# Kernel optimization log

Measured on AMD Instinct MI355X. Metric: run time of the kernel, lower is better.

Reference implementation:

```python
import jax, jax.numpy as jnp
import numpy as np

B, S, D, F, E, K = 4, 2048, 512, 1024, 8, 2

def setup_inputs() -> dict:
    key = jax.random.key(0)
    ks = jax.random.split(key, 7)
    hidden = jax.random.normal(ks[0], (B, S, D), dtype=jnp.float32)
    top_k_indices = jax.random.randint(ks[1], (B, S, K), 0, E, dtype=jnp.int32)
    top_k_weights = jax.random.uniform(ks[2], (B, S, K), dtype=jnp.float32)
    scale1 = 1.0 / np.sqrt(D)
    scale2 = 1.0 / np.sqrt(F)
    W1 = jax.random.normal(ks[3], (E, D, F), dtype=jnp.float32) * scale1
    b1 = jnp.zeros((E, F), dtype=jnp.float32)
    W2 = jax.random.normal(ks[4], (E, F, D), dtype=jnp.float32) * scale2
    b2 = jnp.zeros((E, D), dtype=jnp.float32)
    return {"hidden": hidden, "top_k_indices": top_k_indices,
            "top_k_weights": top_k_weights, "W1": W1, "b1": b1, "W2": W2, "b2": b2}

def reference(hidden, top_k_indices, top_k_weights, W1, b1, W2, b2):
    b, s, d = hidden.shape
    e = W1.shape[0]
    x = hidden.reshape(-1, d)                      # [T, D]
    idx = top_k_indices.reshape(-1, top_k_indices.shape[-1])   # [T, K]
    w = top_k_weights.reshape(-1, top_k_weights.shape[-1])     # [T, K]
    # combine weight per (token, expert): sum over k slots routed to expert e
    onehot = jax.nn.one_hot(idx, e, dtype=w.dtype)             # [T, K, E]
    cw = jnp.einsum('tk,tke->et', w, onehot)                   # [E, T]
    def step(acc, params):
        W1e, b1e, W2e, b2e, cwe = params
        h = jax.nn.gelu(x @ W1e + b1e)                         # [T, F]
        y = h @ W2e + b2e                                      # [T, D]
        return acc + cwe[:, None] * y, None
    out, _ = jax.lax.scan(step, jnp.zeros_like(x), (W1, b1, W2, b2, cw))
    return out.reshape(b, s, d)
```

## Files before the change

kernel.cpp:

```cpp
#include <hip/hip_runtime.h>
#include <hip/hip_bf16.h>

#define T_TOK 8192
#define DDIM  512
#define FDIM  1024
#define NEXP  8
#define KTOP  2
#define NSLOT (T_TOK * KTOP)
#define MAX_ROWS 17408
#define MAX_T128 136

typedef __attribute__((ext_vector_type(8))) __bf16 bf16x8;
typedef __attribute__((ext_vector_type(4))) __bf16 bf16x4;
typedef __attribute__((ext_vector_type(4))) float  f32x4;
typedef __attribute__((ext_vector_type(8))) unsigned short u16x8;

typedef __attribute__((address_space(1))) const unsigned int* gp1;
typedef __attribute__((address_space(3))) unsigned int*       lp3;
#define GL2LDS(g, l) __builtin_amdgcn_global_load_lds((gp1)(const void*)(g), (lp3)(void*)(l), 16, 0, 0)


__device__ __forceinline__ float gelu_fast(float x){
    float u = 0.7978845608028654f * (x + 0.044715f * x * x * x);
    return x / (1.0f + __expf(-2.0f * u));
}

__device__ __forceinline__ unsigned short f2bf(float v){
    __hip_bfloat16 b = __float2bfloat16(v);
    return *(unsigned short*)&b;
}

__global__ void cast_x_bf16(const float* __restrict__ src, unsigned short* __restrict__ dst,
                            int n8){
    int i = blockIdx.x * blockDim.x + threadIdx.x;
    if (i >= n8) return;
    const float4* s = (const float4*)src;
    float4 a = s[2 * i];
    float4 b = s[2 * i + 1];
    u16x8 o;
    o[0] = f2bf(a.x); o[1] = f2bf(a.y); o[2] = f2bf(a.z); o[3] = f2bf(a.w);
    o[4] = f2bf(b.x); o[5] = f2bf(b.y); o[6] = f2bf(b.z); o[7] = f2bf(b.w);
    *(u16x8*)(dst + (size_t)i * 8) = o;
}

__global__ __launch_bounds__(1024) void bucket_kernel(
    const int* __restrict__ idx, int* __restrict__ meta, int2* __restrict__ map,
    int* __restrict__ list, int* __restrict__ slot2row)
{
    __shared__ unsigned long long sA[1024], sB[1024];
    const int tid = threadIdx.x;
    const int base = tid * 16;

    int mye[16];
    unsigned long long a = 0, b = 0;
    #pragma unroll
    for (int i = 0; i < 16; i++){
        int e = idx[base + i] & 7;
        mye[i] = e;
        unsigned long long one = 1ull << (16 * (e & 3));
        if (e < 4) a += one; else b += one;
    }
    sA[tid] = a; sB[tid] = b;
    __syncthreads();

    for (int off = 1; off < 1024; off <<= 1){
        unsigned long long ta = 0, tb = 0;
        if (tid >= off){ ta = sA[tid - off]; tb = sB[tid - off]; }
        __syncthreads();
        sA[tid] += ta; sB[tid] += tb;
        __syncthreads();
    }

    const unsigned long long iA = sA[tid],  iB = sB[tid];
    const unsigned long long tA = sA[1023], tB = sB[1023];

    int cnt[NEXP], pad[NEXP], off_e[NEXP], tc[NEXP + 1];
    tc[0] = 0;
    int o = 0;
    #pragma unroll
    for (int e = 0; e < NEXP; e++){
        unsigned long long src = (e < 4) ? tA : tB;
        cnt[e] = (int)((src >> (16 * (e & 3))) & 0xffffull);
        pad[e] = (cnt[e] + 127) & ~127;
        off_e[e] = o; o += pad[e];
        tc[e + 1] = tc[e] + (pad[e] >> 7);
    }
    const int nrows = o, nt = tc[NEXP];

    if (tid == 0) meta[16] = nt;
    if (tid < NEXP) meta[17 + tid] = off_e[tid];
    if (tid < nt){
        int e = 0;
        while (tid >= tc[e + 1]) e++;
        map[tid] = make_int2(e, off_e[e] + (tid - tc[e]) * 128);
    }

    int run[NEXP];
    #pragma unroll
    for (int e = 0; e < NEXP; e++){
        unsigned long long isrc = (e < 4) ? iA : iB;
        unsigned long long csrc = (e < 4) ? a  : b;
        int incl = (int)((isrc >> (16 * (e & 3))) & 0xffffull);
        int ce   = (int)((csrc >> (16 * (e & 3))) & 0xffffull);
        run[e] = off_e[e] + incl - ce;
    }
    #pragma unroll
    for (int i = 0; i < 16; i++){
        int e = mye[i];
        int gg = run[e]++;
        list[gg] = (base + i) >> 1;
        slot2row[base + i] = gg;
    }

    for (int p = tid; p < nrows; p += 1024){
        #pragma unroll
        for (int e = 0; e < NEXP; e++){
            if (p >= off_e[e] + cnt[e] && p < off_e[e] + pad[e]) list[p] = 0;
        }
    }
}

__global__ void transpose_cast(const float* __restrict__ src,
                               unsigned short* __restrict__ dst, int R, int C){
    __shared__ unsigned short tile[32][33];
    int e = blockIdx.z;
    int c0 = blockIdx.x * 32, r0 = blockIdx.y * 32;
    int tx = threadIdx.x, ty = threadIdx.y;
    const float* sf = src + (size_t)e * R * C;
    unsigned short* d = dst + (size_t)e * R * C;
    #pragma unroll
    for (int i = 0; i < 4; i++)
        tile[ty + i * 8][tx] = f2bf(sf[(size_t)(r0 + ty + i * 8) * C + c0 + tx]);
    __syncthreads();
    #pragma unroll
    for (int i = 0; i < 4; i++)
        d[(size_t)(c0 + ty + i * 8) * R + r0 + tx] = tile[tx][ty + i * 8];
}

#define PIPE_PROLOGUE_SYNC()  do {                                   \
    asm volatile("s_waitcnt vmcnt(0)" ::: "memory");                 \
    __builtin_amdgcn_s_barrier();                                    \
    __builtin_amdgcn_sched_barrier(0);                               \
} while (0)
#define PIPE_STEP_SYNC()  do {                                       \
    __builtin_amdgcn_sched_barrier(0);                               \
    asm volatile("s_waitcnt vmcnt(0) lgkmcnt(0)" ::: "memory");      \
    __builtin_amdgcn_s_barrier();                                    \
    __builtin_amdgcn_sched_barrier(0);                               \
} while (0)

__global__ __launch_bounds__(256, 2) void gemm1_kernel(
    const unsigned short* __restrict__ x,
    const unsigned short* __restrict__ w1t,
    const float* __restrict__ b1,
    const int* __restrict__ meta,
    const int2* __restrict__ map,
    const int* __restrict__ list,
    unsigned short* __restrict__ h)
{
    const int ntiles = meta[16];
    const int nwg = ntiles * (FDIM / 128);
    int id = blockIdx.y * gridDim.x + blockIdx.x;
    if (id >= nwg) return;
    int q = nwg >> 3, r = nwg & 7;
    int xcd = id & 7, rank = id >> 3;
    int swz = (xcd < r) ? (xcd * (q + 1) + rank)
                        : (r * (q + 1) + (xcd - r) * q + rank);
    const int tile = swz >> 3;
    const int n0 = (swz & 7) * 128;
    int2 em = map[tile];
    const int e = em.x, grow0 = em.y;

    __shared__ __align__(16) unsigned short As[2][8192];
    __shared__ __align__(16) unsigned short Bs[2][8192];

    const int tid  = threadIdx.x;
    const int wave = tid >> 6;
    const int lane = tid & 63;
    const int rl   = lane >> 2;
    const int kq   = lane & 3;

    const int row0 = wave * 16 + rl;
    const int row1 = 64 + wave * 16 + rl;

    const unsigned short* pA0 = x + (size_t)list[grow0 + row0] * DDIM + kq * 8;
    const unsigned short* pA1 = x + (size_t)list[grow0 + row1] * DDIM + kq * 8;
    const unsigned short* pB0 = w1t + ((size_t)e * FDIM + n0 + row0) * DDIM + kq * 8;
    const unsigned short* pB1 = w1t + ((size_t)e * FDIM + n0 + row1) * DDIM + kq * 8;

    const int quad = lane >> 4, lrow = lane & 15;
    const int wr = (wave >> 1) * 64;
    const int wc = (wave & 1) * 64;

#define STAGE1(buf, kk) do {                                                  \
        char* la_ = (char*)As[buf] + wave * 1024;                             \
        char* lb_ = (char*)Bs[buf] + wave * 1024;                             \
        GL2LDS(pA0 + (kk),      la_);          GL2LDS(pA1 + (kk),      la_ + 4096);  \
        GL2LDS(pA0 + (kk) + 32, la_ + 8192);   GL2LDS(pA1 + (kk) + 32, la_ + 12288); \
        GL2LDS(pB0 + (kk),      lb_);          GL2LDS(pB1 + (kk),      lb_ + 4096);  \
        GL2LDS(pB0 + (kk) + 32, lb_ + 8192);   GL2LDS(pB1 + (kk) + 32, lb_ + 12288); \
    } while (0)

    f32x4 acc[4][4];
    #pragma unroll
    for (int i = 0; i < 4; i++)
        #pragma unroll
        for (int j = 0; j < 4; j++) acc[i][j] = (f32x4)0.0f;

    STAGE1(0, 0);
    PIPE_PROLOGUE_SYNC();

    const int NK = DDIM / 64;
    #pragma unroll 2
    for (int t = 0; t < NK; ++t){
        const int cur = t & 1;
        if (t + 1 < NK) STAGE1(cur ^ 1, (t + 1) * 64);
        bf16x8 a[4][2], b[4][2];
        #pragma unroll
        for (int i = 0; i < 4; i++){
            #pragma unroll
            for (int ks = 0; ks < 2; ks++){
                a[i][ks] = *(const bf16x8*)&As[cur][ks * 4096 + (wr + i * 16 + lrow) * 32 + quad * 8];
                b[i][ks] = *(const bf16x8*)&Bs[cur][ks * 4096 + (wc + i * 16 + lrow) * 32 + quad * 8];
            }
        }
        #pragma unroll
        for (int i = 0; i < 4; i++){
            #pragma unroll
            for (int j = 0; j < 4; j++){
                acc[i][j] = __builtin_amdgcn_mfma_f32_16x16x32_bf16(a[i][0], b[j][0], acc[i][j], 0, 0, 0);
                acc[i][j] = __builtin_amdgcn_mfma_f32_16x16x32_bf16(a[i][1], b[j][1], acc[i][j], 0, 0, 0);
            }
        }
        if (t + 1 < NK) PIPE_STEP_SYNC();
    }
#undef STAGE1

    #pragma unroll
    for (int j = 0; j < 4; j++){
        int cn = n0 + wc + j * 16 + lrow;
        float bias = b1[e * FDIM + cn];
        #pragma unroll
        for (int i = 0; i < 4; i++){
            #pragma unroll
            for (int rr = 0; rr < 4; rr++){
                int gr = grow0 + wr + i * 16 + quad * 4 + rr;
                h[(size_t)gr * FDIM + cn] = f2bf(gelu_fast(acc[i][j][rr] + bias));
            }
        }
    }
}

__global__ __launch_bounds__(256, 2) void gemm2_kernel(
    const unsigned short* __restrict__ h,
    const unsigned short* __restrict__ w2t,
    const float* __restrict__ b2,
    const int* __restrict__ meta,
    const int2* __restrict__ map,
    unsigned short* __restrict__ y)
{
    const int ntiles = meta[16];
    const int nwg = ntiles * (DDIM / 128);
    int id = blockIdx.y * gridDim.x + blockIdx.x;
    if (id >= nwg) return;
    int q = nwg >> 3, r = nwg & 7;
    int xcd = id & 7, rank = id >> 3;
    int swz = (xcd < r) ? (xcd * (q + 1) + rank)
                        : (r * (q + 1) + (xcd - r) * q + rank);
    const int tile = swz >> 2;
    const int n0 = (swz & 3) * 128;
    int2 em = map[tile];
    const int e = em.x, grow0 = em.y;

    __shared__ __align__(16) unsigned short As[2][8192];
    __shared__ __align__(16) unsigned short Bs[2][8192];

    const int tid  = threadIdx.x;
    const int wave = tid >> 6;
    const int lane = tid & 63;
    const int rl   = lane >> 2;
    const int kq   = lane & 3;

    const int row0 = wave * 16 + rl;
    const int row1 = 64 + wave * 16 + rl;

    const unsigned short* pA0 = h + (size_t)(grow0 + row0) * FDIM + kq * 8;
    const unsigned short* pA1 = h + (size_t)(grow0 + row1) * FDIM + kq * 8;
    const unsigned short* pB0 = w2t + ((size_t)e * DDIM + n0 + row0) * FDIM + kq * 8;
    const unsigned short* pB1 = w2t + ((size_t)e * DDIM + n0 + row1) * FDIM + kq * 8;

    const int quad = lane >> 4, lrow = lane & 15;
    const int wr = (wave >> 1) * 64;
    const int wc = (wave & 1) * 64;

#define STAGE2(buf, kk) do {                                                  \
        char* la_ = (char*)As[buf] + wave * 1024;                             \
        char* lb_ = (char*)Bs[buf] + wave * 1024;                             \
        GL2LDS(pA0 + (kk),      la_);          GL2LDS(pA1 + (kk),      la_ + 4096);  \
        GL2LDS(pA0 + (kk) + 32, la_ + 8192);   GL2LDS(pA1 + (kk) + 32, la_ + 12288); \
        GL2LDS(pB0 + (kk),      lb_);          GL2LDS(pB1 + (kk),      lb_ + 4096);  \
        GL2LDS(pB0 + (kk) + 32, lb_ + 8192);   GL2LDS(pB1 + (kk) + 32, lb_ + 12288); \
    } while (0)

    f32x4 acc[4][4];
    #pragma unroll
    for (int i = 0; i < 4; i++)
        #pragma unroll
        for (int j = 0; j < 4; j++) acc[i][j] = (f32x4)0.0f;

    STAGE2(0, 0);
    PIPE_PROLOGUE_SYNC();

    const int NK = FDIM / 64;
    #pragma unroll 2
    for (int t = 0; t < NK; ++t){
        const int cur = t & 1;
        if (t + 1 < NK) STAGE2(cur ^ 1, (t + 1) * 64);
        bf16x8 a[4][2], b[4][2];
        #pragma unroll
        for (int i = 0; i < 4; i++){
            #pragma unroll
            for (int ks = 0; ks < 2; ks++){
                a[i][ks] = *(const bf16x8*)&As[cur][ks * 4096 + (wr + i * 16 + lrow) * 32 + quad * 8];
                b[i][ks] = *(const bf16x8*)&Bs[cur][ks * 4096 + (wc + i * 16 + lrow) * 32 + quad * 8];
            }
        }
        #pragma unroll
        for (int i = 0; i < 4; i++){
            #pragma unroll
            for (int j = 0; j < 4; j++){
                acc[i][j] = __builtin_amdgcn_mfma_f32_16x16x32_bf16(a[i][0], b[j][0], acc[i][j], 0, 0, 0);
                acc[i][j] = __builtin_amdgcn_mfma_f32_16x16x32_bf16(a[i][1], b[j][1], acc[i][j], 0, 0, 0);
            }
        }
        if (t + 1 < NK) PIPE_STEP_SYNC();
    }
#undef STAGE2

    #pragma unroll
    for (int j = 0; j < 4; j++){
        int cn = n0 + wc + j * 16 + lrow;
        float bias = b2[e * DDIM + cn];
        #pragma unroll
        for (int i = 0; i < 4; i++){
            #pragma unroll
            for (int rr = 0; rr < 4; rr++){
                int gr = grow0 + wr + i * 16 + quad * 4 + rr;
                y[(size_t)gr * DDIM + cn] = f2bf(acc[i][j][rr] + bias);
            }
        }
    }
}

__global__ void combine_kernel(const unsigned short* __restrict__ y,
                               const int* __restrict__ slot2row,
                               const float* __restrict__ wk,
                               float* __restrict__ out){
    int g = blockIdx.x * blockDim.x + threadIdx.x;
    int t = g >> 7, seg = g & 127;
    int ra = slot2row[2 * t], rb = slot2row[2 * t + 1];
    float wa = wk[2 * t];
    float wb = wk[2 * t + 1];
    bf16x4 ya = *(const bf16x4*)(y + (size_t)ra * DDIM + seg * 4);
    bf16x4 yb = *(const bf16x4*)(y + (size_t)rb * DDIM + seg * 4);
    float4 o;
    o.x = wa * (float)ya[0] + wb * (float)yb[0];
    o.y = wa * (float)ya[1] + wb * (float)yb[1];
    o.z = wa * (float)ya[2] + wb * (float)yb[2];
    o.w = wa * (float)ya[3] + wb * (float)yb[3];
    *(float4*)(out + (size_t)t * DDIM + seg * 4) = o;
}

extern "C" void kernel_launch(void* const* d_in, const int* in_sizes, int n_in,
                              void* d_out, int out_size, void* d_ws, size_t ws_size,
                              hipStream_t stream){
    const float* x   = (const float*)d_in[0];
    const int*   idx = (const int*)d_in[1];
    const float* wk  = (const float*)d_in[2];
    const float* W1  = (const float*)d_in[3];
    const float* b1  = (const float*)d_in[4];
    const float* W2  = (const float*)d_in[5];
    const float* b2  = (const float*)d_in[6];
    float* out = (float*)d_out;

    char* ws = (char*)d_ws;
    int*   meta     = (int*)ws;
    int2*  map      = (int2*)(ws + 512);
    int*   list     = (int*)(ws + 4096);
    int*   slot2row = (int*)(ws + 81920);
    unsigned short* xbf = (unsigned short*)(ws + 262144);
    unsigned short* w1t = (unsigned short*)(ws + 8650752);
    unsigned short* w2t = (unsigned short*)(ws + 17039360);
    unsigned short* h   = (unsigned short*)(ws + 25427968);
    unsigned short* y   = (unsigned short*)(ws + 61079552);
    if (ws_size < 78905344u) return;

    cast_x_bf16<<<(T_TOK * DDIM / 8) / 256, 256, 0, stream>>>(x, xbf, T_TOK * DDIM / 8);

    transpose_cast<<<dim3(FDIM / 32, DDIM / 32, NEXP), dim3(32, 8), 0, stream>>>(
        W1, w1t, DDIM, FDIM);
    transpose_cast<<<dim3(DDIM / 32, FDIM / 32, NEXP), dim3(32, 8), 0, stream>>>(
        W2, w2t, FDIM, DDIM);

    bucket_kernel<<<1, 1024, 0, stream>>>(idx, meta, map, list, slot2row);

    gemm1_kernel<<<dim3(FDIM / 128, MAX_T128), 256, 0, stream>>>(
        xbf, w1t, b1, meta, map, list, h);
    gemm2_kernel<<<dim3(DDIM / 128, MAX_T128), 256, 0, stream>>>(
        h, w2t, b2, meta, map, y);

    combine_kernel<<<(T_TOK * DDIM / 4) / 256, 256, 0, stream>>>(y, slot2row, wk, out);
}
```

Baseline: 198.0 us.

## Fuse prep kernels into one launch and shrink GEMM K-tile to 32

Merges the x cast, both weight transpose-casts and the bucketing kernel into a single prep kernel that dispatches on block index, removing three launches. Both grouped GEMMs drop their K step from 64 to 32, halving LDS use per buffer and doubling loop iterations. The step sync no longer waits on lgkmcnt, and the launch_bounds occupancy hint of 2 is removed. The transpose now uses 1024-thread blocks, one element per thread, and the smaller K tile adds more barriers per unit of work.

```diff
diff --git a/kernel.cpp b/kernel.cpp
--- a/kernel.cpp
+++ b/kernel.cpp
@@ -10,6 +10,10 @@
 #define MAX_ROWS 17408
 #define MAX_T128 136
 
+#define NB_CAST 512
+#define NB_T    4096
+#define PREP_BLOCKS (1 + NB_CAST + NB_T + NB_T)
+
 typedef __attribute__((ext_vector_type(8))) __bf16 bf16x8;
 typedef __attribute__((ext_vector_type(4))) __bf16 bf16x4;
 typedef __attribute__((ext_vector_type(4))) float  f32x4;
@@ -30,126 +34,119 @@
     return *(unsigned short*)&b;
 }
 
-__global__ void cast_x_bf16(const float* __restrict__ src, unsigned short* __restrict__ dst,
-                            int n8){
-    int i = blockIdx.x * blockDim.x + threadIdx.x;
-    if (i >= n8) return;
-    const float4* s = (const float4*)src;
-    float4 a = s[2 * i];
-    float4 b = s[2 * i + 1];
-    u16x8 o;
-    o[0] = f2bf(a.x); o[1] = f2bf(a.y); o[2] = f2bf(a.z); o[3] = f2bf(a.w);
-    o[4] = f2bf(b.x); o[5] = f2bf(b.y); o[6] = f2bf(b.z); o[7] = f2bf(b.w);
-    *(u16x8*)(dst + (size_t)i * 8) = o;
-}
-
-__global__ __launch_bounds__(1024) void bucket_kernel(
-    const int* __restrict__ idx, int* __restrict__ meta, int2* __restrict__ map,
+__global__ __launch_bounds__(1024) void prep_kernel(
+    const float* __restrict__ x, const int* __restrict__ idx,
+    const float* __restrict__ W1, const float* __restrict__ W2,
+    unsigned short* __restrict__ xbf,
+    unsigned short* __restrict__ w1t, unsigned short* __restrict__ w2t,
+    int* __restrict__ meta, int2* __restrict__ map,
     int* __restrict__ list, int* __restrict__ slot2row)
 {
     __shared__ unsigned long long sA[1024], sB[1024];
+    __shared__ unsigned short tile[32][33];
+    const int b   = blockIdx.x;
     const int tid = threadIdx.x;
-    const int base = tid * 16;
-
-    int mye[16];
-    unsigned long long a = 0, b = 0;
-    #pragma unroll
-    for (int i = 0; i < 16; i++){
-        int e = idx[base + i] & 7;
-        mye[i] = e;
-        unsigned long long one = 1ull << (16 * (e & 3));
-        if (e < 4) a += one; else b += one;
-    }
-    sA[tid] = a; sB[tid] = b;
-    __syncthreads();
-
-    for (int off = 1; off < 1024; off <<= 1){
-        unsigned long long ta = 0, tb = 0;
-        if (tid >= off){ ta = sA[tid - off]; tb = sB[tid - off]; }
+
+    if (b == 0){
+        const int base = tid * 16;
+        int mye[16];
+        unsigned long long a = 0, bb = 0;
+        #pragma unroll
+        for (int i = 0; i < 16; i++){
+            int e = idx[base + i] & 7;
+            mye[i] = e;
+            unsigned long long one = 1ull << (16 * (e & 3));
+            if (e < 4) a += one; else bb += one;
+        }
+        sA[tid] = a; sB[tid] = bb;
         __syncthreads();
-        sA[tid] += ta; sB[tid] += tb;
+        for (int off = 1; off < 1024; off <<= 1){
+            unsigned long long ta = 0, tb = 0;
+            if (tid >= off){ ta = sA[tid - off]; tb = sB[tid - off]; }
+            __syncthreads();
+            sA[tid] += ta; sB[tid] += tb;
+            __syncthreads();
+        }
+        const unsigned long long iA = sA[tid],  iB = sB[tid];
+        const unsigned long long tA = sA[1023], tB = sB[1023];
+
+        int cnt[NEXP], pad[NEXP], off_e[NEXP], tc[NEXP + 1];
+        tc[0] = 0;
+        int o = 0;
+        #pragma unroll
+        for (int e = 0; e < NEXP; e++){
+            unsigned long long src = (e < 4) ? tA : tB;
+            cnt[e] = (int)((src >> (16 * (e & 3))) & 0xffffull);
+            pad[e] = (cnt[e] + 127) & ~127;
+            off_e[e] = o; o += pad[e];
+            tc[e + 1] = tc[e] + (pad[e] >> 7);
+        }
+        const int nrows = o, nt = tc[NEXP];
+
+        if (tid == 0) meta[16] = nt;
+        if (tid < NEXP) meta[17 + tid] = off_e[tid];
+        if (tid < nt){
+            int e = 0;
+            while (tid >= tc[e + 1]) e++;
+            map[tid] = make_int2(e, off_e[e] + (tid - tc[e]) * 128);
+        }
+
+        int run[NEXP];
+        #pragma unroll
+        for (int e = 0; e < NEXP; e++){
+            unsigned long long isrc = (e < 4) ? iA : iB;
+            unsigned long long csrc = (e < 4) ? a  : bb;
+            int incl = (int)((isrc >> (16 * (e & 3))) & 0xffffull);
+            int ce   = (int)((csrc >> (16 * (e & 3))) & 0xffffull);
+            run[e] = off_e[e] + incl - ce;
+        }
+        #pragma unroll
+        for (int i = 0; i < 16; i++){
+            int e = mye[i];
+            int gg = run[e]++;
+            list[gg] = (base + i) >> 1;
+            slot2row[base + i] = gg;
+        }
+        for (int p = tid; p < nrows; p += 1024){
+            #pragma unroll
+            for (int e = 0; e < NEXP; e++){
+                if (p >= off_e[e] + cnt[e] && p < off_e[e] + pad[e]) list[p] = 0;
+            }
+        }
+    } else if (b < 1 + NB_CAST){
+        int i = (b - 1) * 1024 + tid;
+        const float4* s = (const float4*)x;
+        float4 va = s[2 * i];
+        float4 vb = s[2 * i + 1];
+        u16x8 ov;
+        ov[0] = f2bf(va.x); ov[1] = f2bf(va.y); ov[2] = f2bf(va.z); ov[3] = f2bf(va.w);
+        ov[4] = f2bf(vb.x); ov[5] = f2bf(vb.y); ov[6] = f2bf(vb.z); ov[7] = f2bf(vb.w);
+        *(u16x8*)(xbf + (size_t)i * 8) = ov;
+    } else {
+        int blk = b - (1 + NB_CAST);
+        const float* src; unsigned short* dst; int R, C, cpb_shift, cpb_mask;
+        if (blk < NB_T){ src = W1; dst = w1t; R = DDIM; C = FDIM; cpb_shift = 5; cpb_mask = 31; }
+        else           { src = W2; dst = w2t; R = FDIM; C = DDIM; cpb_shift = 4; cpb_mask = 15; blk -= NB_T; }
+        int e   = blk >> 9;
+        int rem = blk & 511;
+        int rb  = rem >> cpb_shift, cb = rem & cpb_mask;
+        int r0 = rb * 32, c0 = cb * 32;
+        int tx = tid & 31, ty = tid >> 5;
+        const float* sf = src + (size_t)e * R * C;
+        unsigned short* d = dst + (size_t)e * R * C;
+        tile[ty][tx] = f2bf(sf[(size_t)(r0 + ty) * C + c0 + tx]);
         __syncthreads();
-    }
-
-    const unsigned long long iA = sA[tid],  iB = sB[tid];
-    const unsigned long long tA = sA[1023], tB = sB[1023];
-
-    int cnt[NEXP], pad[NEXP], off_e[NEXP], tc[NEXP + 1];
-    tc[0] = 0;
-    int o = 0;
-    #pragma unroll
-    for (int e = 0; e < NEXP; e++){
-        unsigned long long src = (e < 4) ? tA : tB;
-        cnt[e] = (int)((src >> (16 * (e & 3))) & 0xffffull);
-        pad[e] = (cnt[e] + 127) & ~127;
-        off_e[e] = o; o += pad[e];
-        tc[e + 1] = tc[e] + (pad[e] >> 7);
-    }
-    const int nrows = o, nt = tc[NEXP];
-
-    if (tid == 0) meta[16] = nt;
-    if (tid < NEXP) meta[17 + tid] = off_e[tid];
-    if (tid < nt){
-        int e = 0;
-        while (tid >= tc[e + 1]) e++;
-        map[tid] = make_int2(e, off_e[e] + (tid - tc[e]) * 128);
-    }
-
-    int run[NEXP];
-    #pragma unroll
-    for (int e = 0; e < NEXP; e++){
-        unsigned long long isrc = (e < 4) ? iA : iB;
-        unsigned long long csrc = (e < 4) ? a  : b;
-        int incl = (int)((isrc >> (16 * (e & 3))) & 0xffffull);
-        int ce   = (int)((csrc >> (16 * (e & 3))) & 0xffffull);
-        run[e] = off_e[e] + incl - ce;
-    }
-    #pragma unroll
-    for (int i = 0; i < 16; i++){
-        int e = mye[i];
-        int gg = run[e]++;
-        list[gg] = (base + i) >> 1;
-        slot2row[base + i] = gg;
-    }
-
-    for (int p = tid; p < nrows; p += 1024){
-        #pragma unroll
-        for (int e = 0; e < NEXP; e++){
-            if (p >= off_e[e] + cnt[e] && p < off_e[e] + pad[e]) list[p] = 0;
-        }
-    }
-}
-
-__global__ void transpose_cast(const float* __restrict__ src,
-                               unsigned short* __restrict__ dst, int R, int C){
-    __shared__ unsigned short tile[32][33];
-    int e = blockIdx.z;
-    int c0 = blockIdx.x * 32, r0 = blockIdx.y * 32;
-    int tx = threadIdx.x, ty = threadIdx.y;
-    const float* sf = src + (size_t)e * R * C;
-    unsigned short* d = dst + (size_t)e * R * C;
-    #pragma unroll
-    for (int i = 0; i < 4; i++)
-        tile[ty + i * 8][tx] = f2bf(sf[(size_t)(r0 + ty + i * 8) * C + c0 + tx]);
-    __syncthreads();
-    #pragma unroll
-    for (int i = 0; i < 4; i++)
-        d[(size_t)(c0 + ty + i * 8) * R + r0 + tx] = tile[tx][ty + i * 8];
-}
-
-#define PIPE_PROLOGUE_SYNC()  do {                                   \
+        d[(size_t)(c0 + ty) * R + r0 + tx] = tile[tx][ty];
+    }
+}
+
+#define PIPE_SYNC() do {                                             \
     asm volatile("s_waitcnt vmcnt(0)" ::: "memory");                 \
     __builtin_amdgcn_s_barrier();                                    \
     __builtin_amdgcn_sched_barrier(0);                               \
 } while (0)
-#define PIPE_STEP_SYNC()  do {                                       \
-    __builtin_amdgcn_sched_barrier(0);                               \
-    asm volatile("s_waitcnt vmcnt(0) lgkmcnt(0)" ::: "memory");      \
-    __builtin_amdgcn_s_barrier();                                    \
-    __builtin_amdgcn_sched_barrier(0);                               \
-} while (0)
-
-__global__ __launch_bounds__(256, 2) void gemm1_kernel(
+
+__global__ __launch_bounds__(256) void gemm1_kernel(
     const unsigned short* __restrict__ x,
     const unsigned short* __restrict__ w1t,
     const float* __restrict__ b1,
@@ -171,8 +168,8 @@
     int2 em = map[tile];
     const int e = em.x, grow0 = em.y;
 
-    __shared__ __align__(16) unsigned short As[2][8192];
-    __shared__ __align__(16) unsigned short Bs[2][8192];
+    __shared__ __align__(16) unsigned short As[2][128 * 32];
+    __shared__ __align__(16) unsigned short Bs[2][128 * 32];
 
     const int tid  = threadIdx.x;
     const int wave = tid >> 6;
@@ -192,13 +189,11 @@
     const int wr = (wave >> 1) * 64;
     const int wc = (wave & 1) * 64;
 
-#define STAGE1(buf, kk) do {                                                  \
-        char* la_ = (char*)As[buf] + wave * 1024;                             \
-        char* lb_ = (char*)Bs[buf] + wave * 1024;                             \
-        GL2LDS(pA0 + (kk),      la_);          GL2LDS(pA1 + (kk),      la_ + 4096);  \
-        GL2LDS(pA0 + (kk) + 32, la_ + 8192);   GL2LDS(pA1 + (kk) + 32, la_ + 12288); \
-        GL2LDS(pB0 + (kk),      lb_);          GL2LDS(pB1 + (kk),      lb_ + 4096);  \
-        GL2LDS(pB0 + (kk) + 32, lb_ + 8192);   GL2LDS(pB1 + (kk) + 32, lb_ + 12288); \
+#define STG1(buf, kk) do {                                            \
+        char* la_ = (char*)As[buf] + wave * 1024;                     \
+        char* lb_ = (char*)Bs[buf] + wave * 1024;                     \
+        GL2LDS(pA0 + (kk), la_);  GL2LDS(pA1 + (kk), la_ + 4096);     \
+        GL2LDS(pB0 + (kk), lb_);  GL2LDS(pB1 + (kk), lb_ + 4096);     \
     } while (0)
 
     f32x4 acc[4][4];
@@ -207,34 +202,28 @@
         #pragma unroll
         for (int j = 0; j < 4; j++) acc[i][j] = (f32x4)0.0f;
 
-    STAGE1(0, 0);
-    PIPE_PROLOGUE_SYNC();
-
-    const int NK = DDIM / 64;
+    STG1(0, 0);
+    PIPE_SYNC();
+
+    const int NK = DDIM / 32;
     #pragma unroll 2
     for (int t = 0; t < NK; ++t){
         const int cur = t & 1;
-        if (t + 1 < NK) STAGE1(cur ^ 1, (t + 1) * 64);
-        bf16x8 a[4][2], b[4][2];
+        if (t + 1 < NK) STG1(cur ^ 1, (t + 1) * 32);
+        bf16x8 a[4], b[4];
         #pragma unroll
         for (int i = 0; i < 4; i++){
-            #pragma unroll
-            for (int ks = 0; ks < 2; ks++){
-                a[i][ks] = *(const bf16x8*)&As[cur][ks * 4096 + (wr + i * 16 + lrow) * 32 + quad * 8];
-                b[i][ks] = *(const bf16x8*)&Bs[cur][ks * 4096 + (wc + i * 16 + lrow) * 32 + quad * 8];
-            }
-        }
-        #pragma unroll
-        for (int i = 0; i < 4; i++){
-            #pragma unroll
-            for (int j = 0; j < 4; j++){
-                acc[i][j] = __builtin_amdgcn_mfma_f32_16x16x32_bf16(a[i][0], b[j][0], acc[i][j], 0, 0, 0);
-                acc[i][j] = __builtin_amdgcn_mfma_f32_16x16x32_bf16(a[i][1], b[j][1], acc[i][j], 0, 0, 0);
-            }
-        }
-        if (t + 1 < NK) PIPE_STEP_SYNC();
-    }
-#undef STAGE1
+            a[i] = *(const bf16x8*)&As[cur][(wr + i * 16 + lrow) * 32 + quad * 8];
+            b[i] = *(const bf16x8*)&Bs[cur][(wc + i * 16 + lrow) * 32 + quad * 8];
+        }
+        #pragma unroll
+        for (int i = 0; i < 4; i++)
+            #pragma unroll
+            for (int j = 0; j < 4; j++)
+                acc[i][j] = __builtin_amdgcn_mfma_f32_16x16x32_bf16(a[i], b[j], acc[i][j], 0, 0, 0);
+        if (t + 1 < NK) PIPE_SYNC();
+    }
+#undef STG1
 
     #pragma unroll
     for (int j = 0; j < 4; j++){
@@ -251,7 +240,7 @@
     }
 }
 
-__global__ __launch_bounds__(256, 2) void gemm2_kernel(
+__global__ __launch_bounds__(256) void gemm2_kernel(
     const unsigned short* __restrict__ h,
     const unsigned short* __restrict__ w2t,
     const float* __restrict__ b2,
@@ -272,8 +261,8 @@
     int2 em = map[tile];
     const int e = em.x, grow0 = em.y;
 
-    __shared__ __align__(16) unsigned short As[2][8192];
-    __shared__ __align__(16) unsigned short Bs[2][8192];
+    __shared__ __align__(16) unsigned short As[2][128 * 32];
+    __shared__ __align__(16) unsigned short Bs[2][128 * 32];
 
     const int tid  = threadIdx.x;
     const int wave = tid >> 6;
@@ -293,13 +282,11 @@
     const int wr = (wave >> 1) * 64;
     const int wc = (wave & 1) * 64;
 
-#define STAGE2(buf, kk) do {                                                  \
-        char* la_ = (char*)As[buf] + wave * 1024;                             \
-        char* lb_ = (char*)Bs[buf] + wave * 1024;                             \
-        GL2LDS(pA0 + (kk),      la_);          GL2LDS(pA1 + (kk),      la_ + 4096);  \
-        GL2LDS(pA0 + (kk) + 32, la_ + 8192);   GL2LDS(pA1 + (kk) + 32, la_ + 12288); \
-        GL2LDS(pB0 + (kk),      lb_);          GL2LDS(pB1 + (kk),      lb_ + 4096);  \
-        GL2LDS(pB0 + (kk) + 32, lb_ + 8192);   GL2LDS(pB1 + (kk) + 32, lb_ + 12288); \
+#define STG2(buf, kk) do {                                            \
+        char* la_ = (char*)As[buf] + wave * 1024;                     \
+        char* lb_ = (char*)Bs[buf] + wave * 1024;                     \
+        GL2LDS(pA0 + (kk), la_);  GL2LDS(pA1 + (kk), la_ + 4096);     \
+        GL2LDS(pB0 + (kk), lb_);  GL2LDS(pB1 + (kk), lb_ + 4096);     \
     } while (0)
 
     f32x4 acc[4][4];
@@ -308,34 +295,28 @@
         #pragma unroll
         for (int j = 0; j < 4; j++) acc[i][j] = (f32x4)0.0f;
 
-    STAGE2(0, 0);
-    PIPE_PROLOGUE_SYNC();
-
-    const int NK = FDIM / 64;
+    STG2(0, 0);
+    PIPE_SYNC();
+
+    const int NK = FDIM / 32;
     #pragma unroll 2
     for (int t = 0; t < NK; ++t){
         const int cur = t & 1;
-        if (t + 1 < NK) STAGE2(cur ^ 1, (t + 1) * 64);
-        bf16x8 a[4][2], b[4][2];
+        if (t + 1 < NK) STG2(cur ^ 1, (t + 1) * 32);
+        bf16x8 a[4], b[4];
         #pragma unroll
         for (int i = 0; i < 4; i++){
-            #pragma unroll
-            for (int ks = 0; ks < 2; ks++){
-                a[i][ks] = *(const bf16x8*)&As[cur][ks * 4096 + (wr + i * 16 + lrow) * 32 + quad * 8];
-                b[i][ks] = *(const bf16x8*)&Bs[cur][ks * 4096 + (wc + i * 16 + lrow) * 32 + quad * 8];
-            }
-        }
-        #pragma unroll
-        for (int i = 0; i < 4; i++){
-            #pragma unroll
-            for (int j = 0; j < 4; j++){
-                acc[i][j] = __builtin_amdgcn_mfma_f32_16x16x32_bf16(a[i][0], b[j][0], acc[i][j], 0, 0, 0);
-                acc[i][j] = __builtin_amdgcn_mfma_f32_16x16x32_bf16(a[i][1], b[j][1], acc[i][j], 0, 0, 0);
-            }
-        }
-        if (t + 1 < NK) PIPE_STEP_SYNC();
-    }
-#undef STAGE2
+            a[i] = *(const bf16x8*)&As[cur][(wr + i * 16 + lrow) * 32 + quad * 8];
+            b[i] = *(const bf16x8*)&Bs[cur][(wc + i * 16 + lrow) * 32 + quad * 8];
+        }
+        #pragma unroll
+        for (int i = 0; i < 4; i++)
+            #pragma unroll
+            for (int j = 0; j < 4; j++)
+                acc[i][j] = __builtin_amdgcn_mfma_f32_16x16x32_bf16(a[i], b[j], acc[i][j], 0, 0, 0);
+        if (t + 1 < NK) PIPE_SYNC();
+    }
+#undef STG2
 
     #pragma unroll
     for (int j = 0; j < 4; j++){
@@ -395,17 +376,12 @@
     unsigned short* y   = (unsigned short*)(ws + 61079552);
     if (ws_size < 78905344u) return;
 
-    cast_x_bf16<<<(T_TOK * DDIM / 8) / 256, 256, 0, stream>>>(x, xbf, T_TOK * DDIM / 8);
-
-    transpose_cast<<<dim3(FDIM / 32, DDIM / 32, NEXP), dim3(32, 8), 0, stream>>>(
-        W1, w1t, DDIM, FDIM);
-    transpose_cast<<<dim3(DDIM / 32, FDIM / 32, NEXP), dim3(32, 8), 0, stream>>>(
-        W2, w2t, FDIM, DDIM);
-
-    bucket_kernel<<<1, 1024, 0, stream>>>(idx, meta, map, list, slot2row);
+    prep_kernel<<<PREP_BLOCKS, 1024, 0, stream>>>(
+        x, idx, W1, W2, xbf, w1t, w2t, meta, map, list, slot2row);
 
     gemm1_kernel<<<dim3(FDIM / 128, MAX_T128), 256, 0, stream>>>(
         xbf, w1t, b1, meta, map, list, h);
+
     gemm2_kernel<<<dim3(DDIM / 128, MAX_T128), 256, 0, stream>>>(
         h, w2t, b2, meta, map, y);
 
```

New measurement: 210.3 us. 1.06x slower.
